# Performance work log

Hardware: AMD Instinct MI355X
Metric: run time of the kernel (lower is better)

The kernel has to match this reference:

```python
import jax, jax.numpy as jnp
import numpy as np
jax.config.update('jax_enable_x64', True)

B, S, D, H, V, P = 4, 2048, 512, 8, 100000, 256
NGRAMS = list(range(3, 9))  # n-gram lengths 3..8
DH = D // H
SCALE = np.float32(DH ** -0.5)

def _layernorm(x, g, b, eps=1e-5):
    m = jnp.mean(x, -1, keepdims=True)
    v = jnp.mean(jnp.square(x - m), -1, keepdims=True)
    return g * (x - m) / jnp.sqrt(v + eps) + b

def _mha(q, k, v, Wq, bq, Wk, bk, Wv, bv, Wo, bo):
    Bq, Lq, _ = q.shape
    qh = (q @ Wq + bq).reshape(Bq, Lq, H, DH)
    kh = (k @ Wk + bk).reshape(Bq, -1, H, DH)
    vh = (v @ Wv + bv).reshape(Bq, -1, H, DH)
    s = jnp.einsum('bqhd,bkhd->bhqk', qh, kh) * SCALE
    a = jax.nn.softmax(s, axis=-1)
    o = jnp.einsum('bhqk,bkhd->bqhd', a, vh).reshape(Bq, Lq, D)
    return o @ Wo + bo

def _ngram_hash(bytes_seq, n):
    # hash[:, i] = sum_k bytes[:, i-n+1+k] * 256**k for i >= n-1 else 0, then mod V
    # (int64 wraparound for n=8 matches torch semantics)
    b = bytes_seq.astype(jnp.int64)
    h = jnp.zeros_like(b)
    for k in range(n):
        shift = n - 1 - k
        shifted = jnp.pad(b, ((0, 0), (shift, 0)))[:, :S]
        h = h + shifted * (256 ** k)
    h = jnp.where(jnp.arange(S) >= (n - 1), h, 0)
    return h % V

def _forward(bytes_seq, patch_idx, byte_emb, ngram_emb, sWq, sbq, sWk, sbk, sWv, sbv, sWo, sbo, ln1g, ln1b, W1, b1, W2, b2, ln2g, ln2b, cWq, cbq, cWk, cbk, cWv, cbv, cWo, cbo):
    embeds = byte_emb[bytes_seq]  # [B,S,D]
    for j, n in enumerate(NGRAMS):
        embeds = embeds + ngram_emb[j][_ngram_hash(bytes_seq, n)]
    embeds = embeds / np.float32(len(NGRAMS) + 1)
    # one post-norm transformer encoder layer (relu FFN, eval mode / no dropout)
    x = _layernorm(embeds + _mha(embeds, embeds, embeds, sWq, sbq, sWk, sbk, sWv, sbv, sWo, sbo), ln1g, ln1b)
    ff = jax.nn.relu(x @ W1 + b1) @ W2 + b2
    x = _layernorm(x + ff, ln2g, ln2b)
    # gather patch-boundary queries per batch, cross-attend to full sequence
    q = jnp.take_along_axis(x, patch_idx[..., None], axis=1)  # [B,P,D]
    return _mha(q, x, x, cWq, cbq, cWk, cbk, cWv, cbv, cWo, cbo)

def setup_inputs():
    key = jax.random.key(0)
    ks = jax.random.split(key, 20)
    f32 = jnp.float32
    def rn(k, shape, scale=0.02):
        return (jax.random.normal(k, shape, f32) * scale).astype(f32)
    return {
        'bytes_seq': jax.random.randint(ks[0], (B, S), 0, 256, dtype=jnp.int64),
        'patch_idx': jnp.sort(jax.random.randint(ks[1], (B, P), 0, S, dtype=jnp.int64), axis=1),
        'byte_emb': rn(ks[2], (256, D)),
        'ngram_emb': rn(ks[3], (len(NGRAMS), V, D)),
        'sWq': rn(ks[4], (D, D)), 'sbq': jnp.zeros((D,), f32),
        'sWk': rn(ks[5], (D, D)), 'sbk': jnp.zeros((D,), f32),
        'sWv': rn(ks[6], (D, D)), 'sbv': jnp.zeros((D,), f32),
        'sWo': rn(ks[7], (D, D)), 'sbo': jnp.zeros((D,), f32),
        'ln1g': jnp.ones((D,), f32), 'ln1b': jnp.zeros((D,), f32),
        'W1': rn(ks[8], (D, 4 * D)), 'b1': jnp.zeros((4 * D,), f32),
        'W2': rn(ks[9], (4 * D, D)), 'b2': jnp.zeros((D,), f32),
        'ln2g': jnp.ones((D,), f32), 'ln2b': jnp.zeros((D,), f32),
        'cWq': rn(ks[10], (D, D)), 'cbq': jnp.zeros((D,), f32),
        'cWk': rn(ks[11], (D, D)), 'cbk': jnp.zeros((D,), f32),
        'cWv': rn(ks[12], (D, D)), 'cbv': jnp.zeros((D,), f32),
        'cWo': rn(ks[13], (D, D)), 'cbo': jnp.zeros((D,), f32),
    }

def reference(bytes_seq, patch_idx, byte_emb, ngram_emb, sWq, sbq, sWk, sbk, sWv, sbv, sWo, sbo, ln1g, ln1b, W1, b1, W2, b2, ln2g, ln2b, cWq, cbq, cWk, cbk, cWv, cbv, cWo, cbo):
    return _forward(bytes_seq, patch_idx, byte_emb, ngram_emb, sWq, sbq, sWk, sbk, sWv, sbv, sWo, sbo, ln1g, ln1b, W1, b1, W2, b2, ln2g, ln2b, cWq, cbq, cWk, cbk, cWv, cbv, cWo, cbo)
```

## Files before the change

### kernel.cpp

```cpp
#include <hip/hip_runtime.h>
#include <stdint.h>

#define B_   4
#define S_   2048
#define D_   512
#define H_   8
#define DH_  64
#define V_   100000
#define P_   256
#define N_   (B_*S_)
#define NP_  (B_*P_)

typedef _Float16 f16;
typedef _Float16 f16x8 __attribute__((ext_vector_type(8)));
typedef float    f32x4 __attribute__((ext_vector_type(4)));
typedef uint32_t u32x4 __attribute__((ext_vector_type(4)));

#define MFMA16(a,b,c) __builtin_amdgcn_mfma_f32_16x16x32_f16((a),(b),(c),0,0,0)
#define GLDS16(gp, lp) __builtin_amdgcn_global_load_lds( \
    (const __attribute__((address_space(1))) void*)(gp), \
    (__attribute__((address_space(3))) void*)(lp), 16, 0, 0)

__global__ __launch_bounds__(128) void embed_kernel(
    const int* __restrict__ bytes_seq, const float* __restrict__ byte_emb,
    const float* __restrict__ ngram_emb, float* __restrict__ out,
    f16* __restrict__ out16)
{
  const int pos = blockIdx.x;
  const int b = pos / S_, s = pos % S_;
  const int* bs = bytes_seq + (size_t)b * S_;

  int w[8];
  #pragma unroll
  for (int k = 0; k < 8; k++) {
    int p = s - 7 + k;
    w[k] = (p >= 0) ? bs[p] : 0;
  }

  int idx[6];
  #pragma unroll
  for (int j = 0; j < 6; j++) {
    const int n = j + 3;
    int id = 0;
    if (s >= n - 1) {
      uint64_t h = 0;
      for (int k = 0; k < n; k++)
        h += (uint64_t)(uint32_t)w[8 - n + k] << (8 * k);
      long long sh = (long long)h;
      long long r = sh % (long long)V_;
      if (r < 0) r += V_;
      id = (int)r;
    }
    idx[j] = id;
  }

  const int d = threadIdx.x * 4;
  float4 acc = *(const float4*)(byte_emb + (size_t)bs[s] * D_ + d);
  #pragma unroll
  for (int j = 0; j < 6; j++) {
    const float4 v = *(const float4*)(ngram_emb + ((size_t)j * V_ + idx[j]) * D_ + d);
    acc.x += v.x; acc.y += v.y; acc.z += v.z; acc.w += v.w;
  }
  const float inv7 = 1.0f / 7.0f;
  acc.x *= inv7; acc.y *= inv7; acc.z *= inv7; acc.w *= inv7;
  *(float4*)(out + (size_t)pos * D_ + d) = acc;
  f16* o16 = out16 + (size_t)pos * D_ + d;
  o16[0] = (f16)acc.x; o16[1] = (f16)acc.y; o16[2] = (f16)acc.z; o16[3] = (f16)acc.w;
}

struct WJobs {
  const float* src[10];
  f16* dst[10];
  int K[10], N[10], tiles[10];
};

__global__ __launch_bounds__(256) void wconv_kernel(WJobs jobs)
{
  const int j = blockIdx.y;
  const int tile = blockIdx.x;
  if (tile >= jobs.tiles[j]) return;
  const int K = jobs.K[j], N = jobs.N[j];
  const int ntiles = N >> 5;
  const int kt = (tile / ntiles) << 5, nt = (tile % ntiles) << 5;
  __shared__ float T[32][33];
  const int t = threadIdx.x;
  const float* src = jobs.src[j];
  #pragma unroll
  for (int p = 0; p < 4; p++) {
    int lin = t + p * 256;
    int rr = lin >> 5, cc = lin & 31;
    T[rr][cc] = src[(size_t)(kt + rr) * N + nt + cc];
  }
  __syncthreads();
  f16* dst = jobs.dst[j];
  #pragma unroll
  for (int p = 0; p < 4; p++) {
    int lin = t + p * 256;
    int rr = lin >> 5, cc = lin & 31;
    dst[(size_t)(nt + rr) * K + kt + cc] = (f16)T[cc][rr];
  }
}

__global__ __launch_bounds__(256) void bconcat_kernel(
    const float* sbq, const float* sbk, const float* sbv,
    const float* cbk, const float* cbv, float* bqkv, float* bckv)
{
  int t = blockIdx.x * 256 + threadIdx.x;
  if (t < 512)       bqkv[t] = sbq[t];
  else if (t < 1024) bqkv[t] = sbk[t - 512];
  else if (t < 1536) bqkv[t] = sbv[t - 1024];
  else if (t < 2048) bckv[t - 1536] = cbk[t - 1536];
  else if (t < 2560) bckv[t - 1536] = cbv[t - 2048];
}

template<typename OutT, int RELU, int BN>
__global__ __launch_bounds__(256) void gemm_f16(
    const f16* __restrict__ A, const f16* __restrict__ Bt,
    const float* __restrict__ bias, OutT* __restrict__ C,
    int M, int N, int K, const int* __restrict__ rowmap)
{
  constexpr int NF = BN / 32;
  __shared__ __align__(16) f16 As[2][128 * 32];
  __shared__ __align__(16) f16 Bs[2][BN * 32];
  const int tid = threadIdx.x;
  const int l = tid & 63;
  const int lo4 = l & 15, hi2 = l >> 4;
  const int w = tid >> 6;
  const int wr = w >> 1, wc = w & 1;
  const int bm = blockIdx.x * 128, bn = blockIdx.y * BN;

  size_t aoff[2];
  #pragma unroll
  for (int i = 0; i < 2; i++) {
    int r = bm + i * 64 + (tid >> 2);
    int ar = rowmap ? ((r >> 8) * S_ + rowmap[r]) : r;
    aoff[i] = (size_t)ar * K + (tid & 3) * 8;
  }

  f32x4 acc[4][NF];
  #pragma unroll
  for (int m = 0; m < 4; m++)
    #pragma unroll
    for (int n = 0; n < NF; n++) acc[m][n] = (f32x4){0.f, 0.f, 0.f, 0.f};

  const int nt = K >> 5;

  #pragma unroll
  for (int i = 0; i < 2; i++)
    GLDS16(A + aoff[i], &As[0][(i * 256 + tid) * 8]);
  #pragma unroll
  for (int i = 0; i < BN / 64; i++) {
    int c = i * 256 + tid;
    GLDS16(Bt + (size_t)(bn + (c >> 2)) * K + (c & 3) * 8, &Bs[0][c * 8]);
  }

  for (int t = 0; t < nt; t++) {
    __syncthreads();
    const int cur = t & 1;
    if (t + 1 < nt) {
      const int k0 = (t + 1) << 5;
      #pragma unroll
      for (int i = 0; i < 2; i++)
        GLDS16(A + aoff[i] + k0, &As[cur ^ 1][(i * 256 + tid) * 8]);
      #pragma unroll
      for (int i = 0; i < BN / 64; i++) {
        int c = i * 256 + tid;
        GLDS16(Bt + (size_t)(bn + (c >> 2)) * K + k0 + (c & 3) * 8, &Bs[cur ^ 1][c * 8]);
      }
    }
    f16x8 af[4], bf[NF];
    const f16* pa = &As[cur][(wr * 64 + lo4) * 32 + hi2 * 8];
    const f16* pb = &Bs[cur][(wc * (BN / 2) + lo4) * 32 + hi2 * 8];
    #pragma unroll
    for (int m = 0; m < 4; m++) af[m] = *(const f16x8*)(pa + m * 16 * 32);
    #pragma unroll
    for (int n = 0; n < NF; n++) bf[n] = *(const f16x8*)(pb + n * 16 * 32);
    #pragma unroll
    for (int m = 0; m < 4; m++)
      #pragma unroll
      for (int n = 0; n < NF; n++)
        acc[m][n] = MFMA16(af[m], bf[n], acc[m][n]);
  }

  #pragma unroll
  for (int n = 0; n < NF; n++) {
    const int col = bn + wc * (BN / 2) + n * 16 + lo4;
    const float bcol = bias[col];
    #pragma unroll
    for (int m = 0; m < 4; m++) {
      const int row0 = bm + wr * 64 + m * 16 + hi2 * 4;
      #pragma unroll
      for (int j = 0; j < 4; j++) {
        float v = acc[m][n][j] + bcol;
        if (RELU) v = fmaxf(v, 0.f);
        C[(size_t)(row0 + j) * N + col] = (OutT)v;
      }
    }
  }
}

__global__ __launch_bounds__(256) void attn_f16(
    const f16* __restrict__ Q, int qs,
    const f16* __restrict__ Kp, const f16* __restrict__ Vp, int kvs,
    f16* __restrict__ O, int NQ)
{
  __shared__ __align__(16) f16 Ks[2][64][76];
  __shared__ __align__(16) f16 Vt[2][64][76];

  const int tid = threadIdx.x;
  const int w = tid >> 6, l = tid & 63;
  const int lo4 = l & 15, hi2 = l >> 4;
  const int lin = blockIdx.x;
  const int h = lin & 7, b = (lin >> 3) & 3, qt = lin >> 5;

  const int qrow = qt * 64 + w * 16 + lo4;
  const f16* Qp = Q + (size_t)(b * NQ + qrow) * qs + h * DH_ + hi2 * 8;
  f16x8 qf[2];
  qf[0] = *(const f16x8*)(Qp);
  qf[1] = *(const f16x8*)(Qp + 32);
  const f16 qscale = (f16)0.18033688f;
  #pragma unroll
  for (int i = 0; i < 8; i++) { qf[0][i] *= qscale; qf[1][i] *= qscale; }

  const int g2 = lo4 >> 2, j4 = lo4 & 3;
  const int kvp0 = 8 * g2 + j4;
  const int kvp1 = 8 * (g2 ^ 2) + 4 + j4;
  const int pidx = (l ^ 32) << 2;

  const f16* Kb = Kp + (size_t)b * S_ * kvs + h * DH_;
  const f16* Vb = Vp + (size_t)b * S_ * kvs + h * DH_;

  float lsum = 0.f;
  f32x4 oacc[4];
  #pragma unroll
  for (int df = 0; df < 4; df++) oacc[df] = (f32x4){0.f, 0.f, 0.f, 0.f};

  const int r0 = tid >> 3;
  const int c8 = tid & 7;

  f16x8 kreg[2], vreg[2];
  #pragma unroll
  for (int i = 0; i < 2; i++) {
    int row = i * 32 + r0;
    kreg[i] = *(const f16x8*)(Kb + (size_t)row * kvs + c8 * 8);
    vreg[i] = *(const f16x8*)(Vb + (size_t)row * kvs + c8 * 8);
  }
  #pragma unroll
  for (int i = 0; i < 2; i++) {
    int row = i * 32 + r0;
    *(f16x8*)(&Ks[0][row][c8 * 8]) = kreg[i];
    #pragma unroll
    for (int jj = 0; jj < 8; jj++) Vt[0][c8 * 8 + jj][row] = vreg[i][jj];
  }
  __syncthreads();

  const int NT = S_ / 64;
  int cur = 0;
  for (int t = 0; t < NT; t++) {
    if (t + 1 < NT) {
      #pragma unroll
      for (int i = 0; i < 2; i++) {
        int row = (t + 1) * 64 + i * 32 + r0;
        kreg[i] = *(const f16x8*)(Kb + (size_t)row * kvs + c8 * 8);
        vreg[i] = *(const f16x8*)(Vb + (size_t)row * kvs + c8 * 8);
      }
    }
    f32x4 sacc[4];
    #pragma unroll
    for (int nf = 0; nf < 4; nf++) {
      const int krow = ((nf & 1) ? kvp1 : kvp0) + (nf >> 1) * 32;
      f32x4 s = (f32x4){0.f, 0.f, 0.f, 0.f};
      f16x8 kf0 = *(const f16x8*)(&Ks[cur][krow][hi2 * 8]);
      f16x8 kf1 = *(const f16x8*)(&Ks[cur][krow][32 + hi2 * 8]);
      s = MFMA16(kf0, qf[0], s);
      s = MFMA16(kf1, qf[1], s);
      sacc[nf] = s;
    }
    uint32_t packs[4][2];
    #pragma unroll
    for (int nf = 0; nf < 4; nf++) {
      float p0 = exp2f(fminf(sacc[nf][0], 15.f));
      float p1 = exp2f(fminf(sacc[nf][1], 15.f));
      float p2 = exp2f(fminf(sacc[nf][2], 15.f));
      float p3 = exp2f(fminf(sacc[nf][3], 15.f));
      lsum += (p0 + p1) + (p2 + p3);
      packs[nf][0] = __builtin_bit_cast(uint32_t, __builtin_amdgcn_cvt_pkrtz(p0, p1));
      packs[nf][1] = __builtin_bit_cast(uint32_t, __builtin_amdgcn_cvt_pkrtz(p2, p3));
    }
    #pragma unroll
    for (int ks = 0; ks < 2; ks++) {
      uint32_t w0 = packs[2 * ks][0];
      uint32_t w1 = packs[2 * ks][1];
      uint32_t w2 = (uint32_t)__builtin_amdgcn_ds_bpermute(pidx, (int)packs[2 * ks + 1][0]);
      uint32_t w3 = (uint32_t)__builtin_amdgcn_ds_bpermute(pidx, (int)packs[2 * ks + 1][1]);
      u32x4 bw = (u32x4){w0, w1, w2, w3};
      f16x8 pb = __builtin_bit_cast(f16x8, bw);
      #pragma unroll
      for (int df = 0; df < 4; df++) {
        f16x8 vf = *(const f16x8*)(&Vt[cur][df * 16 + lo4][ks * 32 + hi2 * 8]);
        oacc[df] = MFMA16(vf, pb, oacc[df]);
      }
    }
    if (t + 1 < NT) {
      #pragma unroll
      for (int i = 0; i < 2; i++) {
        int row = i * 32 + r0;
        *(f16x8*)(&Ks[cur ^ 1][row][c8 * 8]) = kreg[i];
        #pragma unroll
        for (int jj = 0; jj < 8; jj++) Vt[cur ^ 1][c8 * 8 + jj][row] = vreg[i][jj];
      }
    }
    __syncthreads();
    cur ^= 1;
  }

  lsum += __shfl_xor(lsum, 16, 64);
  lsum += __shfl_xor(lsum, 32, 64);
  const float invl = 1.0f / lsum;

  const int orow = qt * 64 + w * 16 + lo4;
  f16* Ob = O + (size_t)(b * NQ + orow) * D_ + h * DH_ + hi2 * 4;
  #pragma unroll
  for (int df = 0; df < 4; df++) {
    f16 t4[4];
    #pragma unroll
    for (int j = 0; j < 4; j++) t4[j] = (f16)(oacc[df][j] * invl);
    *(uint2*)(Ob + df * 16) = *(uint2*)t4;
  }
}

__global__ __launch_bounds__(128) void ln_kernel(
    const float* __restrict__ a, const float* __restrict__ r,
    const float* __restrict__ g, const float* __restrict__ be,
    float* __restrict__ out, f16* __restrict__ out16)
{
  const int row = blockIdx.x;
  const int t = threadIdx.x;
  const float4 va = *(const float4*)(a + (size_t)row * D_ + t * 4);
  const float4 vr = *(const float4*)(r + (size_t)row * D_ + t * 4);
  const float x0 = va.x + vr.x, x1 = va.y + vr.y, x2 = va.z + vr.z, x3 = va.w + vr.w;
  float sm = x0 + x1 + x2 + x3;
  float sq = x0*x0 + x1*x1 + x2*x2 + x3*x3;
  #pragma unroll
  for (int off = 32; off > 0; off >>= 1) {
    sm += __shfl_down(sm, off, 64);
    sq += __shfl_down(sq, off, 64);
  }
  __shared__ float s0[2], s1[2];
  if ((t & 63) == 0) { s0[t >> 6] = sm; s1[t >> 6] = sq; }
  __syncthreads();
  const float Sm = s0[0] + s0[1];
  const float Sq = s1[0] + s1[1];
  const float mean = Sm * (1.0f / 512.0f);
  const float var  = Sq * (1.0f / 512.0f) - mean * mean;
  const float inv  = rsqrtf(var + 1e-5f);
  const float4 vg = *(const float4*)(g + t * 4);
  const float4 vb = *(const float4*)(be + t * 4);
  float4 o;
  o.x = vg.x * (x0 - mean) * inv + vb.x;
  o.y = vg.y * (x1 - mean) * inv + vb.y;
  o.z = vg.z * (x2 - mean) * inv + vb.z;
  o.w = vg.w * (x3 - mean) * inv + vb.w;
  *(float4*)(out + (size_t)row * D_ + t * 4) = o;
  f16* o16 = out16 + (size_t)row * D_ + t * 4;
  o16[0] = (f16)o.x; o16[1] = (f16)o.y; o16[2] = (f16)o.z; o16[3] = (f16)o.w;
}

extern "C" void kernel_launch(void* const* d_in, const int* in_sizes, int n_in,
                              void* d_out, int out_size, void* d_ws, size_t ws_size,
                              hipStream_t stream) {
  const int*   bytes_seq = (const int*)  d_in[0];
  const int*   patch_idx = (const int*)  d_in[1];
  const float* byte_emb  = (const float*)d_in[2];
  const float* ngram_emb = (const float*)d_in[3];
  const float* sWq = (const float*)d_in[4];  const float* sbq = (const float*)d_in[5];
  const float* sWk = (const float*)d_in[6];  const float* sbk = (const float*)d_in[7];
  const float* sWv = (const float*)d_in[8];  const float* sbv = (const float*)d_in[9];
  const float* sWo = (const float*)d_in[10]; const float* sbo = (const float*)d_in[11];
  const float* ln1g = (const float*)d_in[12]; const float* ln1b = (const float*)d_in[13];
  const float* W1 = (const float*)d_in[14];  const float* b1 = (const float*)d_in[15];
  const float* W2 = (const float*)d_in[16];  const float* b2 = (const float*)d_in[17];
  const float* ln2g = (const float*)d_in[18]; const float* ln2b = (const float*)d_in[19];
  const float* cWq = (const float*)d_in[20]; const float* cbq = (const float*)d_in[21];
  const float* cWk = (const float*)d_in[22]; const float* cbk = (const float*)d_in[23];
  const float* cWv = (const float*)d_in[24]; const float* cbv = (const float*)d_in[25];
  const float* cWo = (const float*)d_in[26]; const float* cbo = (const float*)d_in[27];

  char* base = (char*)d_ws;
  const size_t MB = 1u << 20;
  float* E     = (float*)(base + 0 * MB);
  float* TMP   = (float*)(base + 16 * MB);
  float* X1    = (float*)(base + 32 * MB);
  f16* E16     = (f16*)(base + 48 * MB);
  f16* X116    = (f16*)(base + 56 * MB);
  f16* X216    = (f16*)(base + 64 * MB);
  f16* QKV16   = (f16*)(base + 72 * MB);
  f16* AT16    = (f16*)(base + 96 * MB);
  f16* HID16   = (f16*)(base + 104 * MB);
  f16* CKV16   = (f16*)(base + 136 * MB);
  f16* CQ16    = (f16*)(base + 152 * MB);
  f16* CO16    = (f16*)(base + 153 * MB);
  f16* WT      = (f16*)(base + 160 * MB);
  float* bqkv  = (float*)(base + 170 * MB);
  float* bckv  = bqkv + 1536;

  f16* QKVT = WT;
  f16* sWoT = QKVT + 786432;
  f16* W1T  = sWoT + 262144;
  f16* W2T  = W1T + 1048576;
  f16* cWqT = W2T + 1048576;
  f16* CKVT = cWqT + 262144;
  f16* cWoT = CKVT + 524288;

  WJobs wj;
  {
    const float* wsrc[10] = {sWq, sWk, sWv, sWo, W1, W2, cWq, cWk, cWv, cWo};
    f16* wdst[10] = {QKVT, QKVT + 262144, QKVT + 524288, sWoT, W1T, W2T,
                     cWqT, CKVT, CKVT + 262144, cWoT};
    const int wK[10] = {512,512,512,512, 512,2048, 512,512,512,512};
    const int wN[10] = {512,512,512,512, 2048,512, 512,512,512,512};
    for (int i = 0; i < 10; i++) {
      wj.src[i] = wsrc[i]; wj.dst[i] = wdst[i];
      wj.K[i] = wK[i]; wj.N[i] = wN[i];
      wj.tiles[i] = (wK[i] >> 5) * (wN[i] >> 5);
    }
  }

  const dim3 blk256(256), blk128(128);

  wconv_kernel<<<dim3(1024, 10), blk256, 0, stream>>>(wj);
  bconcat_kernel<<<10, blk256, 0, stream>>>(sbq, sbk, sbv, cbk, cbv, bqkv, bckv);
  embed_kernel<<<N_, blk128, 0, stream>>>(bytes_seq, byte_emb, ngram_emb, E, E16);

  gemm_f16<f16, 0, 128><<<dim3(64, 12), blk256, 0, stream>>>(E16, QKVT, bqkv, QKV16, N_, 1536, 512, nullptr);

  attn_f16<<<1024, blk256, 0, stream>>>(QKV16, 1536, QKV16 + 512, QKV16 + 1024, 1536, AT16, S_);

  gemm_f16<float, 0, 64><<<dim3(64, 8), blk256, 0, stream>>>(AT16, sWoT, sbo, TMP, N_, 512, 512, nullptr);
  ln_kernel<<<N_, blk128, 0, stream>>>(E, TMP, ln1g, ln1b, X1, X116);

  gemm_f16<f16, 1, 128><<<dim3(64, 16), blk256, 0, stream>>>(X116, W1T, b1, HID16, N_, 2048, 512, nullptr);
  gemm_f16<float, 0, 64><<<dim3(64, 8), blk256, 0, stream>>>(HID16, W2T, b2, TMP, N_, 512, 2048, nullptr);
  ln_kernel<<<N_, blk128, 0, stream>>>(X1, TMP, ln2g, ln2b, E , X216);

  gemm_f16<f16, 0, 128><<<dim3(64, 8), blk256, 0, stream>>>(X216, CKVT, bckv, CKV16, N_, 1024, 512, nullptr);
  gemm_f16<f16, 0, 64><<<dim3(8, 8), blk256, 0, stream>>>(X216, cWqT, cbq, CQ16, NP_, 512, 512, patch_idx);
  attn_f16<<<128, blk256, 0, stream>>>(CQ16, 512, CKV16, CKV16 + 512, 1024, CO16, P_);

  gemm_f16<float, 0, 64><<<dim3(8, 8), blk256, 0, stream>>>(CO16, cWoT, cbo, (float*)d_out, NP_, 512, 512, nullptr);
}
```

Measured before the change: 336.1 us.

## Drop fp32 intermediates, fuse bias concat, and process two query tiles per attention block

The embed, residual-GEMM and layernorm buffers now use fp16 only, replacing fp32 copies and halving their memory traffic. The bias-concat kernel is folded into the weight-conversion launch, which saves one launch. Self-attention now handles two 16-row query groups per warp (QG=2), so each K/V tile loaded into shared memory is reused twice, with half as many blocks. The trade-off is lower precision in the residual path, higher register pressure, and fewer blocks to fill the CUs.

```diff
diff --git a/kernel.cpp b/kernel.cpp
--- a/kernel.cpp
+++ b/kernel.cpp
@@ -23,8 +23,7 @@
 
 __global__ __launch_bounds__(128) void embed_kernel(
     const int* __restrict__ bytes_seq, const float* __restrict__ byte_emb,
-    const float* __restrict__ ngram_emb, float* __restrict__ out,
-    f16* __restrict__ out16)
+    const float* __restrict__ ngram_emb, f16* __restrict__ out16)
 {
   const int pos = blockIdx.x;
   const int b = pos / S_, s = pos % S_;
@@ -62,10 +61,11 @@
     acc.x += v.x; acc.y += v.y; acc.z += v.z; acc.w += v.w;
   }
   const float inv7 = 1.0f / 7.0f;
-  acc.x *= inv7; acc.y *= inv7; acc.z *= inv7; acc.w *= inv7;
-  *(float4*)(out + (size_t)pos * D_ + d) = acc;
   f16* o16 = out16 + (size_t)pos * D_ + d;
-  o16[0] = (f16)acc.x; o16[1] = (f16)acc.y; o16[2] = (f16)acc.z; o16[3] = (f16)acc.w;
+  f16 t4[4];
+  t4[0] = (f16)(acc.x * inv7); t4[1] = (f16)(acc.y * inv7);
+  t4[2] = (f16)(acc.z * inv7); t4[3] = (f16)(acc.w * inv7);
+  *(uint2*)o16 = *(uint2*)t4;
 }
 
 struct WJobs {
@@ -74,10 +74,21 @@
   int K[10], N[10], tiles[10];
 };
 
-__global__ __launch_bounds__(256) void wconv_kernel(WJobs jobs)
+__global__ __launch_bounds__(256) void wconv_kernel(WJobs jobs,
+    const float* sbq, const float* sbk, const float* sbv,
+    const float* cbk, const float* cbv, float* bqkv, float* bckv)
 {
   const int j = blockIdx.y;
   const int tile = blockIdx.x;
+  if (j == 0 && tile >= jobs.tiles[0] && tile < jobs.tiles[0] + 10) {
+    int t = (tile - jobs.tiles[0]) * 256 + threadIdx.x;
+    if (t < 512)       bqkv[t] = sbq[t];
+    else if (t < 1024) bqkv[t] = sbk[t - 512];
+    else if (t < 1536) bqkv[t] = sbv[t - 1024];
+    else if (t < 2048) bckv[t - 1536] = cbk[t - 1536];
+    else if (t < 2560) bckv[t - 1536] = cbv[t - 2048];
+    return;
+  }
   if (tile >= jobs.tiles[j]) return;
   const int K = jobs.K[j], N = jobs.N[j];
   const int ntiles = N >> 5;
@@ -99,18 +110,6 @@
     int rr = lin >> 5, cc = lin & 31;
     dst[(size_t)(nt + rr) * K + kt + cc] = (f16)T[cc][rr];
   }
-}
-
-__global__ __launch_bounds__(256) void bconcat_kernel(
-    const float* sbq, const float* sbk, const float* sbv,
-    const float* cbk, const float* cbv, float* bqkv, float* bckv)
-{
-  int t = blockIdx.x * 256 + threadIdx.x;
-  if (t < 512)       bqkv[t] = sbq[t];
-  else if (t < 1024) bqkv[t] = sbk[t - 512];
-  else if (t < 1536) bqkv[t] = sbv[t - 1024];
-  else if (t < 2048) bckv[t - 1536] = cbk[t - 1536];
-  else if (t < 2560) bckv[t - 1536] = cbv[t - 2048];
 }
 
 template<typename OutT, int RELU, int BN>
@@ -199,6 +198,7 @@
   }
 }
 
+template<int QG>
 __global__ __launch_bounds__(256) void attn_f16(
     const f16* __restrict__ Q, int qs,
     const f16* __restrict__ Kp, const f16* __restrict__ Vp, int kvs,
@@ -213,14 +213,17 @@
   const int lin = blockIdx.x;
   const int h = lin & 7, b = (lin >> 3) & 3, qt = lin >> 5;
 
-  const int qrow = qt * 64 + w * 16 + lo4;
-  const f16* Qp = Q + (size_t)(b * NQ + qrow) * qs + h * DH_ + hi2 * 8;
-  f16x8 qf[2];
-  qf[0] = *(const f16x8*)(Qp);
-  qf[1] = *(const f16x8*)(Qp + 32);
   const f16 qscale = (f16)0.18033688f;
-  #pragma unroll
-  for (int i = 0; i < 8; i++) { qf[0][i] *= qscale; qf[1][i] *= qscale; }
+  f16x8 qf[QG][2];
+  #pragma unroll
+  for (int qg = 0; qg < QG; qg++) {
+    const int qrow = qt * (64 * QG) + w * (16 * QG) + qg * 16 + lo4;
+    const f16* Qp = Q + (size_t)(b * NQ + qrow) * qs + h * DH_ + hi2 * 8;
+    qf[qg][0] = *(const f16x8*)(Qp);
+    qf[qg][1] = *(const f16x8*)(Qp + 32);
+    #pragma unroll
+    for (int i = 0; i < 8; i++) { qf[qg][0][i] *= qscale; qf[qg][1][i] *= qscale; }
+  }
 
   const int g2 = lo4 >> 2, j4 = lo4 & 3;
   const int kvp0 = 8 * g2 + j4;
@@ -230,10 +233,14 @@
   const f16* Kb = Kp + (size_t)b * S_ * kvs + h * DH_;
   const f16* Vb = Vp + (size_t)b * S_ * kvs + h * DH_;
 
-  float lsum = 0.f;
-  f32x4 oacc[4];
-  #pragma unroll
-  for (int df = 0; df < 4; df++) oacc[df] = (f32x4){0.f, 0.f, 0.f, 0.f};
+  float lsum[QG];
+  f32x4 oacc[QG][4];
+  #pragma unroll
+  for (int qg = 0; qg < QG; qg++) {
+    lsum[qg] = 0.f;
+    #pragma unroll
+    for (int df = 0; df < 4; df++) oacc[qg][df] = (f32x4){0.f, 0.f, 0.f, 0.f};
+  }
 
   const int r0 = tid >> 3;
   const int c8 = tid & 7;
@@ -265,40 +272,51 @@
         vreg[i] = *(const f16x8*)(Vb + (size_t)row * kvs + c8 * 8);
       }
     }
-    f32x4 sacc[4];
+    f32x4 sacc[QG][4];
     #pragma unroll
     for (int nf = 0; nf < 4; nf++) {
       const int krow = ((nf & 1) ? kvp1 : kvp0) + (nf >> 1) * 32;
-      f32x4 s = (f32x4){0.f, 0.f, 0.f, 0.f};
       f16x8 kf0 = *(const f16x8*)(&Ks[cur][krow][hi2 * 8]);
       f16x8 kf1 = *(const f16x8*)(&Ks[cur][krow][32 + hi2 * 8]);
-      s = MFMA16(kf0, qf[0], s);
-      s = MFMA16(kf1, qf[1], s);
-      sacc[nf] = s;
-    }
-    uint32_t packs[4][2];
-    #pragma unroll
-    for (int nf = 0; nf < 4; nf++) {
-      float p0 = exp2f(fminf(sacc[nf][0], 15.f));
-      float p1 = exp2f(fminf(sacc[nf][1], 15.f));
-      float p2 = exp2f(fminf(sacc[nf][2], 15.f));
-      float p3 = exp2f(fminf(sacc[nf][3], 15.f));
-      lsum += (p0 + p1) + (p2 + p3);
-      packs[nf][0] = __builtin_bit_cast(uint32_t, __builtin_amdgcn_cvt_pkrtz(p0, p1));
-      packs[nf][1] = __builtin_bit_cast(uint32_t, __builtin_amdgcn_cvt_pkrtz(p2, p3));
-    }
+      #pragma unroll
+      for (int qg = 0; qg < QG; qg++) {
+        f32x4 s = (f32x4){0.f, 0.f, 0.f, 0.f};
+        s = MFMA16(kf0, qf[qg][0], s);
+        s = MFMA16(kf1, qf[qg][1], s);
+        sacc[qg][nf] = s;
+      }
+    }
+    uint32_t packs[QG][4][2];
+    #pragma unroll
+    for (int qg = 0; qg < QG; qg++)
+      #pragma unroll
+      for (int nf = 0; nf < 4; nf++) {
+        float p0 = exp2f(fminf(sacc[qg][nf][0], 15.f));
+        float p1 = exp2f(fminf(sacc[qg][nf][1], 15.f));
+        float p2 = exp2f(fminf(sacc[qg][nf][2], 15.f));
+        float p3 = exp2f(fminf(sacc[qg][nf][3], 15.f));
+        lsum[qg] += (p0 + p1) + (p2 + p3);
+        packs[qg][nf][0] = __builtin_bit_cast(uint32_t, __builtin_amdgcn_cvt_pkrtz(p0, p1));
+        packs[qg][nf][1] = __builtin_bit_cast(uint32_t, __builtin_amdgcn_cvt_pkrtz(p2, p3));
+      }
     #pragma unroll
     for (int ks = 0; ks < 2; ks++) {
-      uint32_t w0 = packs[2 * ks][0];
-      uint32_t w1 = packs[2 * ks][1];
-      uint32_t w2 = (uint32_t)__builtin_amdgcn_ds_bpermute(pidx, (int)packs[2 * ks + 1][0]);
-      uint32_t w3 = (uint32_t)__builtin_amdgcn_ds_bpermute(pidx, (int)packs[2 * ks + 1][1]);
-      u32x4 bw = (u32x4){w0, w1, w2, w3};
-      f16x8 pb = __builtin_bit_cast(f16x8, bw);
+      f16x8 pb[QG];
+      #pragma unroll
+      for (int qg = 0; qg < QG; qg++) {
+        uint32_t w0 = packs[qg][2 * ks][0];
+        uint32_t w1 = packs[qg][2 * ks][1];
+        uint32_t w2 = (uint32_t)__builtin_amdgcn_ds_bpermute(pidx, (int)packs[qg][2 * ks + 1][0]);
+        uint32_t w3 = (uint32_t)__builtin_amdgcn_ds_bpermute(pidx, (int)packs[qg][2 * ks + 1][1]);
+        u32x4 bw = (u32x4){w0, w1, w2, w3};
+        pb[qg] = __builtin_bit_cast(f16x8, bw);
+      }
       #pragma unroll
       for (int df = 0; df < 4; df++) {
         f16x8 vf = *(const f16x8*)(&Vt[cur][df * 16 + lo4][ks * 32 + hi2 * 8]);
-        oacc[df] = MFMA16(vf, pb, oacc[df]);
+        #pragma unroll
+        for (int qg = 0; qg < QG; qg++)
+          oacc[qg][df] = MFMA16(vf, pb[qg], oacc[qg][df]);
       }
     }
     if (t + 1 < NT) {
@@ -314,31 +332,40 @@
     cur ^= 1;
   }
 
-  lsum += __shfl_xor(lsum, 16, 64);
-  lsum += __shfl_xor(lsum, 32, 64);
-  const float invl = 1.0f / lsum;
-
-  const int orow = qt * 64 + w * 16 + lo4;
-  f16* Ob = O + (size_t)(b * NQ + orow) * D_ + h * DH_ + hi2 * 4;
-  #pragma unroll
-  for (int df = 0; df < 4; df++) {
-    f16 t4[4];
-    #pragma unroll
-    for (int j = 0; j < 4; j++) t4[j] = (f16)(oacc[df][j] * invl);
-    *(uint2*)(Ob + df * 16) = *(uint2*)t4;
+  #pragma unroll
+  for (int qg = 0; qg < QG; qg++) {
+    float r = lsum[qg];
+    r += __shfl_xor(r, 16, 64);
+    r += __shfl_xor(r, 32, 64);
+    const float invl = 1.0f / r;
+    const int orow = qt * (64 * QG) + w * (16 * QG) + qg * 16 + lo4;
+    f16* Ob = O + (size_t)(b * NQ + orow) * D_ + h * DH_ + hi2 * 4;
+    #pragma unroll
+    for (int df = 0; df < 4; df++) {
+      f16 t4[4];
+      #pragma unroll
+      for (int j = 0; j < 4; j++) t4[j] = (f16)(oacc[qg][df][j] * invl);
+      *(uint2*)(Ob + df * 16) = *(uint2*)t4;
+    }
   }
 }
 
 __global__ __launch_bounds__(128) void ln_kernel(
-    const float* __restrict__ a, const float* __restrict__ r,
+    const f16* __restrict__ a, const f16* __restrict__ r,
     const float* __restrict__ g, const float* __restrict__ be,
-    float* __restrict__ out, f16* __restrict__ out16)
+    f16* __restrict__ out)
 {
   const int row = blockIdx.x;
   const int t = threadIdx.x;
-  const float4 va = *(const float4*)(a + (size_t)row * D_ + t * 4);
-  const float4 vr = *(const float4*)(r + (size_t)row * D_ + t * 4);
-  const float x0 = va.x + vr.x, x1 = va.y + vr.y, x2 = va.z + vr.z, x3 = va.w + vr.w;
+  const f16* ap = a + (size_t)row * D_ + t * 4;
+  const f16* rp = r + (size_t)row * D_ + t * 4;
+  uint2 au = *(const uint2*)ap, ru = *(const uint2*)rp;
+  f16 a4[4], r4[4];
+  *(uint2*)a4 = au; *(uint2*)r4 = ru;
+  float x0 = (float)a4[0] + (float)r4[0];
+  float x1 = (float)a4[1] + (float)r4[1];
+  float x2 = (float)a4[2] + (float)r4[2];
+  float x3 = (float)a4[3] + (float)r4[3];
   float sm = x0 + x1 + x2 + x3;
   float sq = x0*x0 + x1*x1 + x2*x2 + x3*x3;
   #pragma unroll
@@ -356,14 +383,12 @@
   const float inv  = rsqrtf(var + 1e-5f);
   const float4 vg = *(const float4*)(g + t * 4);
   const float4 vb = *(const float4*)(be + t * 4);
-  float4 o;
-  o.x = vg.x * (x0 - mean) * inv + vb.x;
-  o.y = vg.y * (x1 - mean) * inv + vb.y;
-  o.z = vg.z * (x2 - mean) * inv + vb.z;
-  o.w = vg.w * (x3 - mean) * inv + vb.w;
-  *(float4*)(out + (size_t)row * D_ + t * 4) = o;
-  f16* o16 = out16 + (size_t)row * D_ + t * 4;
-  o16[0] = (f16)o.x; o16[1] = (f16)o.y; o16[2] = (f16)o.z; o16[3] = (f16)o.w;
+  f16 o4[4];
+  o4[0] = (f16)(vg.x * (x0 - mean) * inv + vb.x);
+  o4[1] = (f16)(vg.y * (x1 - mean) * inv + vb.y);
+  o4[2] = (f16)(vg.z * (x2 - mean) * inv + vb.z);
+  o4[3] = (f16)(vg.w * (x3 - mean) * inv + vb.w);
+  *(uint2*)(out + (size_t)row * D_ + t * 4) = *(uint2*)o4;
 }
 
 extern "C" void kernel_launch(void* const* d_in, const int* in_sizes, int n_in,
@@ -388,20 +413,18 @@
 
   char* base = (char*)d_ws;
   const size_t MB = 1u << 20;
-  float* E     = (float*)(base + 0 * MB);
-  float* TMP   = (float*)(base + 16 * MB);
-  float* X1    = (float*)(base + 32 * MB);
-  f16* E16     = (f16*)(base + 48 * MB);
-  f16* X116    = (f16*)(base + 56 * MB);
-  f16* X216    = (f16*)(base + 64 * MB);
-  f16* QKV16   = (f16*)(base + 72 * MB);
-  f16* AT16    = (f16*)(base + 96 * MB);
-  f16* HID16   = (f16*)(base + 104 * MB);
-  f16* CKV16   = (f16*)(base + 136 * MB);
-  f16* CQ16    = (f16*)(base + 152 * MB);
-  f16* CO16    = (f16*)(base + 153 * MB);
-  f16* WT      = (f16*)(base + 160 * MB);
-  float* bqkv  = (float*)(base + 170 * MB);
+  f16* E16     = (f16*)(base + 0 * MB);
+  f16* TMP16   = (f16*)(base + 8 * MB);
+  f16* X116    = (f16*)(base + 16 * MB);
+  f16* X216    = (f16*)(base + 24 * MB);
+  f16* QKV16   = (f16*)(base + 32 * MB);
+  f16* AT16    = (f16*)(base + 56 * MB);
+  f16* HID16   = (f16*)(base + 64 * MB);
+  f16* CKV16   = (f16*)(base + 96 * MB);
+  f16* CQ16    = (f16*)(base + 112 * MB);
+  f16* CO16    = (f16*)(base + 113 * MB);
+  f16* WT      = (f16*)(base + 114 * MB);
+  float* bqkv  = (float*)(base + 123 * MB);
   float* bckv  = bqkv + 1536;
 
   f16* QKVT = WT;
@@ -428,24 +451,23 @@
 
   const dim3 blk256(256), blk128(128);
 
-  wconv_kernel<<<dim3(1024, 10), blk256, 0, stream>>>(wj);
-  bconcat_kernel<<<10, blk256, 0, stream>>>(sbq, sbk, sbv, cbk, cbv, bqkv, bckv);
-  embed_kernel<<<N_, blk128, 0, stream>>>(bytes_seq, byte_emb, ngram_emb, E, E16);
+  wconv_kernel<<<dim3(1024, 10), blk256, 0, stream>>>(wj, sbq, sbk, sbv, cbk, cbv, bqkv, bckv);
+  embed_kernel<<<N_, blk128, 0, stream>>>(bytes_seq, byte_emb, ngram_emb, E16);
 
   gemm_f16<f16, 0, 128><<<dim3(64, 12), blk256, 0, stream>>>(E16, QKVT, bqkv, QKV16, N_, 1536, 512, nullptr);
 
-  attn_f16<<<1024, blk256, 0, stream>>>(QKV16, 1536, QKV16 + 512, QKV16 + 1024, 1536, AT16, S_);
-
-  gemm_f16<float, 0, 64><<<dim3(64, 8), blk256, 0, stream>>>(AT16, sWoT, sbo, TMP, N_, 512, 512, nullptr);
-  ln_kernel<<<N_, blk128, 0, stream>>>(E, TMP, ln1g, ln1b, X1, X116);
+  attn_f16<2><<<512, blk256, 0, stream>>>(QKV16, 1536, QKV16 + 512, QKV16 + 1024, 1536, AT16, S_);
+
+  gemm_f16<f16, 0, 64><<<dim3(64, 8), blk256, 0, stream>>>(AT16, sWoT, sbo, TMP16, N_, 512, 512, nullptr);
+  ln_kernel<<<N_, blk128, 0, stream>>>(E16, TMP16, ln1g, ln1b, X116);
 
   gemm_f16<f16, 1, 128><<<dim3(64, 16), blk256, 0, stream>>>(X116, W1T, b1, HID16, N_, 2048, 512, nullptr);
-  gemm_f16<float, 0, 64><<<dim3(64, 8), blk256, 0, stream>>>(HID16, W2T, b2, TMP, N_, 512, 2048, nullptr);
-  ln_kernel<<<N_, blk128, 0, stream>>>(X1, TMP, ln2g, ln2b, E , X216);
+  gemm_f16<f16, 0, 64><<<dim3(64, 8), blk256, 0, stream>>>(HID16, W2T, b2, TMP16, N_, 512, 2048, nullptr);
+  ln_kernel<<<N_, blk128, 0, stream>>>(X116, TMP16, ln2g, ln2b, X216);
 
   gemm_f16<f16, 0, 128><<<dim3(64, 8), blk256, 0, stream>>>(X216, CKVT, bckv, CKV16, N_, 1024, 512, nullptr);
   gemm_f16<f16, 0, 64><<<dim3(8, 8), blk256, 0, stream>>>(X216, cWqT, cbq, CQ16, NP_, 512, 512, patch_idx);
-  attn_f16<<<128, blk256, 0, stream>>>(CQ16, 512, CKV16, CKV16 + 512, 1024, CO16, P_);
+  attn_f16<1><<<128, blk256, 0, stream>>>(CQ16, 512, CKV16, CKV16 + 512, 1024, CO16, P_);
 
   gemm_f16<float, 0, 64><<<dim3(8, 8), blk256, 0, stream>>>(CO16, cWoT, cbo, (float*)d_out, NP_, 512, 512, nullptr);
 }
```

Result: faster. 287.4 us (-14.5%).
